# Kernel optimization log

Measured on AMD Instinct MI355X. Metric: run time of the kernel, lower is better.

## Reference

```python
import jax, jax.numpy as jnp
import numpy as np

N = 100000
E = 1600000
D = 64
NEG_SLOPE = 0.2


def setup_inputs() -> dict:
    key = jax.random.key(0)
    ks = jax.random.split(key, 16)
    inp = {}
    inp['x'] = jax.random.normal(ks[0], (N, D), dtype=jnp.float32)
    for i, name in enumerate(['edges_pos_out', 'edges_pos_in', 'edges_neg_out', 'edges_neg_in']):
        inp[name] = jax.random.randint(ks[1 + i], (2, E), 0, N, dtype=jnp.int64)
    s = 1.0 / np.sqrt(D)
    inp['gat_W'] = jax.random.normal(ks[5], (2, 4, D, D), dtype=jnp.float32) * s
    inp['gat_att_src'] = jax.random.normal(ks[6], (2, 4, D), dtype=jnp.float32) * s
    inp['gat_att_dst'] = jax.random.normal(ks[7], (2, 4, D), dtype=jnp.float32) * s
    inp['gat_bias'] = jnp.zeros((2, 4, D), dtype=jnp.float32)
    inp['mlp_W1'] = jax.random.normal(ks[8], (2, 5 * D, D), dtype=jnp.float32) * (1.0 / np.sqrt(5 * D))
    inp['mlp_b1'] = jnp.zeros((2, D), dtype=jnp.float32)
    inp['mlp_W2'] = jax.random.normal(ks[9], (2, D, D), dtype=jnp.float32) * s
    inp['mlp_b2'] = jnp.zeros((2, D), dtype=jnp.float32)
    return inp


def _gat(x, W, att_src, att_dst, bias, src, dst):
    # PyG GATConv, heads=1, add_self_loops=True
    n = x.shape[0]
    h = x @ W                                  # [N, D]
    a_src = h @ att_src                        # [N]
    a_dst = h @ att_dst                        # [N]
    loops = jnp.arange(n, dtype=src.dtype)
    s = jnp.concatenate([src, loops])
    d = jnp.concatenate([dst, loops])
    alpha = jax.nn.leaky_relu(a_src[s] + a_dst[d], NEG_SLOPE)   # [E+N]
    m = jax.ops.segment_max(alpha, d, num_segments=n)
    e = jnp.exp(alpha - m[d])
    z = jax.ops.segment_sum(e, d, num_segments=n)
    w = e / z[d]
    out = jax.ops.segment_sum(w[:, None] * h[s], d, num_segments=n)
    return out + bias


def _sdr_layer(x, edge_lists, W, a_s, a_d, b, W1, b1, W2, b2):
    feats = [x]
    for r, (src, dst) in enumerate(edge_lists):
        feats.append(_gat(x, W[r], a_s[r], a_d[r], b[r], src, dst))
    combined = jnp.concatenate(feats, axis=1)          # [N, 5D]
    hidden = jnp.tanh(combined @ W1 + b1)
    return hidden @ W2 + b2


def reference(x, edges_pos_out, edges_pos_in, edges_neg_out, edges_neg_in,
              gat_W, gat_att_src, gat_att_dst, gat_bias,
              mlp_W1, mlp_b1, mlp_W2, mlp_b2):
    edge_lists = [(e[0], e[1]) for e in
                  (edges_pos_out, edges_pos_in, edges_neg_out, edges_neg_in)]
    for l in range(gat_W.shape[0]):
        x = _sdr_layer(x, edge_lists, gat_W[l], gat_att_src[l], gat_att_dst[l],
                       gat_bias[l], mlp_W1[l], mlp_b1[l], mlp_W2[l], mlp_b2[l])
    return x
```

## Files before the change

### kernel.cpp

```cpp
#include <hip/hip_runtime.h>
#include <hip/hip_bf16.h>
#include <math.h>

#define D 64
#define NEG 0.2f
#define WPB 4
#define BLK 256
#define DPB 128
#define MAXNB 1024
#define CHUNK 16384

typedef __attribute__((ext_vector_type(8))) short bf8;
typedef __attribute__((ext_vector_type(4))) float f4;
typedef __attribute__((ext_vector_type(4))) int i4;

__device__ __forceinline__ float lrelu(float v) { return v > 0.f ? v : NEG * v; }

__device__ __forceinline__ unsigned short f2bf(float f) {
    unsigned u = __float_as_uint(f);
    u = (u + 0x7fffu + ((u >> 16) & 1u)) >> 16;
    return (unsigned short)u;
}
__device__ __forceinline__ bf8 ld_frag_g(const unsigned short* p) {
    i4 v = *(const i4*)p;
    return __builtin_bit_cast(bf8, v);
}

__device__ __forceinline__ const int* edge_ptr(const int* e0, const int* e1,
                                               const int* e2, const int* e3, int r)
{
    return (r == 0) ? e0 : (r == 1) ? e1 : (r == 2) ? e2 : e3;
}


__global__ __launch_bounds__(256) void k_bcount(
    const int* __restrict__ e0, const int* __restrict__ e1,
    const int* __restrict__ e2, const int* __restrict__ e3,
    int* __restrict__ bcnt, int E, int NB)
{
    int r = blockIdx.y;
    const int* dst = edge_ptr(e0, e1, e2, e3, r) + E;
    __shared__ int hist[MAXNB];
    for (int i = threadIdx.x; i < NB; i += 256) hist[i] = 0;
    __syncthreads();
    int base = blockIdx.x * CHUNK;
    int end = base + CHUNK < E ? base + CHUNK : E;
    for (int i = base + threadIdx.x; i < end; i += 256)
        atomicAdd(&hist[dst[i] >> 7], 1);
    __syncthreads();
    for (int i = threadIdx.x; i < NB; i += 256)
        if (hist[i]) atomicAdd(&bcnt[r * NB + i], hist[i]);
}

__global__ __launch_bounds__(1024) void k_bscan(
    const int* __restrict__ bcnt, int* __restrict__ boff,
    int* __restrict__ bcur, int* __restrict__ prefix, int E, int N, int NB)
{
    int r = blockIdx.y;
    __shared__ int sh[1024];
    int t = threadIdx.x;
    int v = (t < NB) ? bcnt[r * NB + t] : 0;
    sh[t] = v;
    __syncthreads();
    for (int off = 1; off < 1024; off <<= 1) {
        int add = (t >= off) ? sh[t - off] : 0;
        __syncthreads();
        sh[t] += add;
        __syncthreads();
    }
    if (t < NB) {
        int excl = sh[t] - v;
        boff[r * (NB + 1) + t] = excl;
        bcur[r * NB + t] = excl;
    }
    if (t == 0) {
        boff[r * (NB + 1) + NB] = E;
        prefix[(size_t)r * (N + 1) + N] = E;
    }
}

__global__ __launch_bounds__(256) void k_part(
    const int* __restrict__ e0, const int* __restrict__ e1,
    const int* __restrict__ e2, const int* __restrict__ e3,
    int* __restrict__ gcur, unsigned* __restrict__ staging, int E, int NB)
{
    int r = blockIdx.y;
    const int* ep = edge_ptr(e0, e1, e2, e3, r);
    const int* srcp = ep;
    const int* dstp = ep + E;
    __shared__ int hist[MAXNB];
    __shared__ int base[MAXNB];
    for (int j = threadIdx.x; j < NB; j += 256) hist[j] = 0;
    __syncthreads();
    int begin = blockIdx.x * CHUNK;
    int end = begin + CHUNK < E ? begin + CHUNK : E;
    for (int i = begin + threadIdx.x; i < end; i += 256)
        atomicAdd(&hist[dstp[i] >> 7], 1);
    __syncthreads();
    for (int j = threadIdx.x; j < NB; j += 256) {
        int c = hist[j];
        base[j] = c ? atomicAdd(&gcur[r * NB + j], c) : 0;
        hist[j] = 0;
    }
    __syncthreads();
    unsigned* stg = staging + (size_t)r * E;
    for (int i = begin + threadIdx.x; i < end; i += 256) {
        int d = dstp[i];
        int b = d >> 7;
        int pos = base[b] + atomicAdd(&hist[b], 1);
        stg[pos] = ((unsigned)srcp[i] << 7) | (unsigned)(d & 127);
    }
}

__global__ __launch_bounds__(256) void k_place(
    const unsigned* __restrict__ staging, const int* __restrict__ boff,
    int* __restrict__ prefix, int* __restrict__ srcs, int N, int E, int NB)
{
    int r = blockIdx.y;
    int b = blockIdx.x;
    int t = threadIdx.x;
    __shared__ int lcount[DPB];
    __shared__ int ls[DPB];
    __shared__ int lcur[DPB];
    int gbase = boff[r * (NB + 1) + b];
    int bcnt = boff[r * (NB + 1) + b + 1] - gbase;
    if (t < DPB) lcount[t] = 0;
    __syncthreads();
    const unsigned* st = staging + (size_t)r * E + gbase;
    for (int i = t; i < bcnt; i += 256)
        atomicAdd(&lcount[st[i] & 127], 1);
    __syncthreads();
    if (t < DPB) ls[t] = lcount[t];
    __syncthreads();
    for (int off = 1; off < DPB; off <<= 1) {
        int add = (t < DPB && t >= off) ? ls[t - off] : 0;
        __syncthreads();
        if (t < DPB) ls[t] += add;
        __syncthreads();
    }
    int lo = b * DPB;
    if (t < DPB) {
        int excl = ls[t] - lcount[t];
        lcur[t] = excl;
        int d = lo + t;
        if (d < N) prefix[(size_t)r * (N + 1) + d] = gbase + excl;
    }
    __syncthreads();
    for (int i = t; i < bcnt; i += 256) {
        unsigned v = st[i];
        int pos = atomicAdd(&lcur[v & 127], 1);
        srcs[(size_t)r * E + gbase + pos] = (int)(v >> 7);
    }
}


__global__ __launch_bounds__(256) void k_xcast(
    const float* __restrict__ x, unsigned short* __restrict__ xb, int n4)
{
    int i = blockIdx.x * 256 + threadIdx.x;
    if (i < n4) {
        float4 v = ((const float4*)x)[i];
        ushort4 o;
        o.x = f2bf(v.x); o.y = f2bf(v.y); o.z = f2bf(v.z); o.w = f2bf(v.w);
        ((ushort4*)xb)[i] = o;
    }
}

__global__ __launch_bounds__(64) void k_pack(
    const float* __restrict__ gatW, const float* __restrict__ atS,
    const float* __restrict__ atD, const float* __restrict__ W1,
    const float* __restrict__ W2, unsigned short* __restrict__ WgP,
    unsigned short* __restrict__ W1P, unsigned short* __restrict__ W2P)
{
    int f = blockIdx.x;
    int L = threadIdx.x;
    int kg = L >> 4, c = L & 15;
    unsigned short vals[8];
    unsigned short* dst;
    if (f < 80) {
        int m = f / 10, rem = f % 10;
        int l = m / 4, r = m % 4;
        int kc = rem / 5, ct = rem % 5;
        const float* W = gatW + (size_t)(l * 4 + r) * D * D;
        if (ct < 4) {
#pragma unroll
            for (int j = 0; j < 8; j++) {
                int k = kc * 32 + kg * 8 + j;
                vals[j] = f2bf(W[k * D + ct * 16 + c]);
            }
        } else {
            const float* att = (c == 0) ? atS + (size_t)(l * 4 + r) * D
                                        : atD + (size_t)(l * 4 + r) * D;
#pragma unroll
            for (int j = 0; j < 8; j++) {
                int k = kc * 32 + kg * 8 + j;
                float s = 0.f;
                if (c < 2)
                    for (int cc = 0; cc < D; cc++) s += W[k * D + cc] * att[cc];
                vals[j] = f2bf(s);
            }
        }
        dst = WgP + ((size_t)f * 64 + L) * 8;
    } else if (f < 160) {
        int f2 = f - 80;
        int l = f2 / 40, rem = f2 % 40;
        int kc = rem / 4, ct = rem % 4;
        const float* W = W1 + (size_t)l * 5 * D * D;
#pragma unroll
        for (int j = 0; j < 8; j++) {
            int k = kc * 32 + kg * 8 + j;
            vals[j] = f2bf(W[k * D + ct * 16 + c]);
        }
        dst = W1P + ((size_t)f2 * 64 + L) * 8;
    } else {
        int f3 = f - 160;
        int l = f3 / 8, rem = f3 % 8;
        int kc = rem / 4, ct = rem % 4;
        const float* W = W2 + (size_t)l * D * D;
#pragma unroll
        for (int j = 0; j < 8; j++) {
            int k = kc * 32 + kg * 8 + j;
            vals[j] = f2bf(W[k * D + ct * 16 + c]);
        }
        dst = W2P + ((size_t)f3 * 64 + L) * 8;
    }
    i4 v = __builtin_bit_cast(i4, *(bf8*)vals);
    *(i4*)dst = v;
}


__device__ __forceinline__ void gemm_h_body(
    bf8 a0, bf8 a1, const unsigned short* __restrict__ WgPl,
    unsigned short* __restrict__ h, float* __restrict__ a_s,
    float* __restrict__ a_d, int n0, int kg, int lo, int L, int N)
{
#pragma unroll
    for (int r = 0; r < 4; r++) {
        const unsigned short* Wbase = WgPl + (size_t)r * 10 * 512;
#pragma unroll
        for (int ct = 0; ct < 5; ct++) {
            f4 acc = {0.f, 0.f, 0.f, 0.f};
            bf8 b0 = ld_frag_g(Wbase + (size_t)ct * 512 + (size_t)L * 8);
            bf8 b1 = ld_frag_g(Wbase + (size_t)(5 + ct) * 512 + (size_t)L * 8);
            acc = __builtin_amdgcn_mfma_f32_16x16x32_bf16(a0, b0, acc, 0, 0, 0);
            acc = __builtin_amdgcn_mfma_f32_16x16x32_bf16(a1, b1, acc, 0, 0, 0);
#pragma unroll
            for (int q = 0; q < 4; q++) {
                int node = n0 + kg * 4 + q;
                if (node < N) {
                    if (ct < 4)
                        h[((size_t)r * N + node) * D + ct * 16 + lo] = f2bf(acc[q]);
                    else if (lo == 0)
                        a_s[(size_t)r * N + node] = acc[q];
                    else if (lo == 1)
                        a_d[(size_t)r * N + node] = acc[q];
                }
            }
        }
    }
}

__global__ __launch_bounds__(BLK) void k_gemm_h(
    const unsigned short* __restrict__ xb, const unsigned short* __restrict__ WgPl,
    unsigned short* __restrict__ h, float* __restrict__ a_s,
    float* __restrict__ a_d, int N)
{
    int w = threadIdx.x >> 6, L = threadIdx.x & 63;
    int n0 = blockIdx.x * 64 + w * 16;
    int lo = L & 15, kg = L >> 4;
    int nA = n0 + lo; if (nA >= N) nA = N - 1;
    bf8 a0 = ld_frag_g(xb + (size_t)nA * D + kg * 8);
    bf8 a1 = ld_frag_g(xb + (size_t)nA * D + 32 + kg * 8);
    gemm_h_body(a0, a1, WgPl, h, a_s, a_d, n0, kg, lo, L, N);
}

__global__ __launch_bounds__(BLK) void k_agg(
    const unsigned short* __restrict__ h, const float* __restrict__ a_sall,
    const float* __restrict__ a_dall, const int* __restrict__ prefix,
    const int* __restrict__ srcsall, const float* __restrict__ gatB,
    unsigned short* __restrict__ g, int N, int E)
{
    __shared__ int2 pairs[WPB][64];
    int r = blockIdx.y;
    int w = threadIdx.x >> 6, lane = threadIdx.x & 63;
    int half = lane >> 5, fl = lane & 31;
    int d = (blockIdx.x * WPB + w) * 2 + half;
    if (d >= N) d = N - 1;

    const unsigned short* hr = h + (size_t)r * N * D;
    const float* a_src = a_sall + (size_t)r * N;
    const int* starts = prefix + (size_t)r * (N + 1);
    const int* srcs = srcsall + (size_t)r * E;

    int base = starts[d];
    int cnt = starts[d + 1] - base;
    float ad = a_dall[(size_t)r * N + d];

    float e_self = __expf(lrelu(a_src[d] + ad));
    float zpart = (fl == 0) ? e_self : 0.f;
    float accx, accy;
    {
        unsigned u = ((const unsigned*)(hr + (size_t)d * D))[fl];
        accx = e_self * __uint_as_float(u << 16);
        accy = e_self * __uint_as_float(u & 0xffff0000u);
    }

    int cntmax = max(cnt, __shfl_xor(cnt, 32));
    for (int c0 = 0; c0 < cntmax; c0 += 32) {
        int jj = c0 + fl;
        bool valid = jj < cnt;
        int s = valid ? srcs[base + jj] : 0;
        float e = valid ? __expf(lrelu(a_src[s] + ad)) : 0.f;
        zpart += e;
        pairs[w][lane] = make_int2(s * (int)(D * 2), __float_as_int(e));
        __threadfence_block();
        int lim = cntmax - c0; if (lim > 32) lim = 32;
        int rlim = (lim + 3) & ~3;
#pragma unroll 2
        for (int t = 0; t < rlim; t += 2) {
            i4 pv = *(const i4*)(&pairs[w][half * 32 + t]);
            unsigned uA = *(const unsigned*)((const char*)hr + pv.x + fl * 4);
            unsigned uB = *(const unsigned*)((const char*)hr + pv.z + fl * 4);
            float eA = __int_as_float(pv.y), eB = __int_as_float(pv.w);
            accx = fmaf(eA, __uint_as_float(uA << 16), accx);
            accy = fmaf(eA, __uint_as_float(uA & 0xffff0000u), accy);
            accx = fmaf(eB, __uint_as_float(uB << 16), accx);
            accy = fmaf(eB, __uint_as_float(uB & 0xffff0000u), accy);
        }
        __threadfence_block();
    }

    float z = zpart;
#pragma unroll
    for (int off = 16; off; off >>= 1) z += __shfl_xor(z, off);

    float rz = 1.f / z;
    float vlo = accx * rz + gatB[r * D + 2 * fl];
    float vhi = accy * rz + gatB[r * D + 2 * fl + 1];
    unsigned o = (unsigned)f2bf(vlo) | ((unsigned)f2bf(vhi) << 16);
    ((unsigned*)g)[((size_t)r * N + d) * 32 + fl] = o;
}

__global__ __launch_bounds__(BLK) void k_mlp(
    const unsigned short* __restrict__ xb, const unsigned short* __restrict__ g,
    const unsigned short* __restrict__ W1Pl, const float* __restrict__ b1l,
    const unsigned short* __restrict__ W2Pl, const float* __restrict__ b2l,
    void* __restrict__ outp, int N, int last,
    const unsigned short* __restrict__ WgPn, unsigned short* __restrict__ hn,
    float* __restrict__ a_sn, float* __restrict__ a_dn)
{
    __shared__ unsigned short sh[WPB][16 * 80];
    int w = threadIdx.x >> 6, L = threadIdx.x & 63;
    int n0 = blockIdx.x * 64 + w * 16;
    int lo = L & 15, kg = L >> 4;
    int nA = n0 + lo; if (nA >= N) nA = N - 1;

    f4 acc[4];
#pragma unroll
    for (int ct = 0; ct < 4; ct++) acc[ct] = (f4){0.f, 0.f, 0.f, 0.f};

#pragma unroll
    for (int p = 0; p < 5; p++) {
        const unsigned short* plane = (p == 0) ? xb : g + (size_t)(p - 1) * N * D;
#pragma unroll
        for (int kc2 = 0; kc2 < 2; kc2++) {
            bf8 a = ld_frag_g(plane + (size_t)nA * D + kc2 * 32 + kg * 8);
            int kc = p * 2 + kc2;
#pragma unroll
            for (int ct = 0; ct < 4; ct++) {
                bf8 b = ld_frag_g(W1Pl + ((size_t)(kc * 4 + ct) * 512 + (size_t)L * 8));
                acc[ct] = __builtin_amdgcn_mfma_f32_16x16x32_bf16(a, b, acc[ct], 0, 0, 0);
            }
        }
    }

    unsigned short* tile = &sh[w][0];
#pragma unroll
    for (int ct = 0; ct < 4; ct++) {
        float bb = b1l[ct * 16 + lo];
#pragma unroll
        for (int q = 0; q < 4; q++)
            tile[(kg * 4 + q) * 80 + ct * 16 + lo] = f2bf(tanhf(acc[ct][q] + bb));
    }
    __syncthreads();

    f4 o[4];
#pragma unroll
    for (int ct = 0; ct < 4; ct++) o[ct] = (f4){0.f, 0.f, 0.f, 0.f};
#pragma unroll
    for (int kc = 0; kc < 2; kc++) {
        const unsigned short* ap = tile + lo * 80 + kc * 32 + kg * 8;
        i4 av = *(const i4*)ap;
        bf8 a = __builtin_bit_cast(bf8, av);
#pragma unroll
        for (int ct = 0; ct < 4; ct++) {
            bf8 b = ld_frag_g(W2Pl + ((size_t)(kc * 4 + ct) * 512 + (size_t)L * 8));
            o[ct] = __builtin_amdgcn_mfma_f32_16x16x32_bf16(a, b, o[ct], 0, 0, 0);
        }
    }
    __syncthreads();
#pragma unroll
    for (int ct = 0; ct < 4; ct++) {
        float bb = b2l[ct * 16 + lo];
#pragma unroll
        for (int q = 0; q < 4; q++) {
            int node = n0 + kg * 4 + q;
            int col = ct * 16 + lo;
            float v = o[ct][q] + bb;
            if (node < N) {
                if (last) ((float*)outp)[(size_t)node * D + col] = v;
                else ((unsigned short*)outp)[(size_t)node * D + col] = f2bf(v);
            }
            if (!last) tile[(kg * 4 + q) * 80 + col] = f2bf(v);
        }
    }
    if (last) return;

    __syncthreads();
    bf8 a0, a1;
    {
        i4 v0 = *(const i4*)(tile + lo * 80 + kg * 8);
        i4 v1 = *(const i4*)(tile + lo * 80 + 32 + kg * 8);
        a0 = __builtin_bit_cast(bf8, v0);
        a1 = __builtin_bit_cast(bf8, v1);
    }
    gemm_h_body(a0, a1, WgPn, hn, a_sn, a_dn, n0, kg, lo, L, N);
}


extern "C" void kernel_launch(void* const* d_in, const int* in_sizes, int n_in,
                              void* d_out, int out_size, void* d_ws, size_t ws_size,
                              hipStream_t stream)
{
    const float* x    = (const float*)d_in[0];
    const int*   e0   = (const int*)d_in[1];
    const int*   e1   = (const int*)d_in[2];
    const int*   e2   = (const int*)d_in[3];
    const int*   e3   = (const int*)d_in[4];
    const float* gatW = (const float*)d_in[5];
    const float* atS  = (const float*)d_in[6];
    const float* atD  = (const float*)d_in[7];
    const float* gatB = (const float*)d_in[8];
    const float* W1   = (const float*)d_in[9];
    const float* b1   = (const float*)d_in[10];
    const float* W2   = (const float*)d_in[11];
    const float* b2   = (const float*)d_in[12];
    float* out = (float*)d_out;

    const int N = in_sizes[0] / D;
    const int E = in_sizes[1] / 2;
    const int NB = (N + DPB - 1) / DPB;

    size_t off = 0;
    auto alloc = [&](size_t bytes) { size_t o = off; off = (off + bytes + 255) & ~(size_t)255; return o; };
    unsigned short* xb    = (unsigned short*)((char*)d_ws + alloc((size_t)N * D * 2));
    unsigned short* xnext = (unsigned short*)((char*)d_ws + alloc((size_t)N * D * 2));
    unsigned short* h     = (unsigned short*)((char*)d_ws + alloc((size_t)4 * N * D * 2));
    unsigned short* g     = (unsigned short*)((char*)d_ws + alloc((size_t)4 * N * D * 2));
    unsigned* staging = (unsigned*)g;
    float* a_s   = (float*)((char*)d_ws + alloc((size_t)4 * N * 4));
    float* a_d   = (float*)((char*)d_ws + alloc((size_t)4 * N * 4));
    int* prefix  = (int*)((char*)d_ws + alloc((size_t)4 * (N + 1) * 4));
    int* srcs    = (int*)((char*)d_ws + alloc((size_t)4 * E * 4));
    int* bcnt    = (int*)((char*)d_ws + alloc((size_t)4 * NB * 4));
    int* boff    = (int*)((char*)d_ws + alloc((size_t)4 * (NB + 1) * 4));
    int* bcur    = (int*)((char*)d_ws + alloc((size_t)4 * NB * 4));
    unsigned short* WgP = (unsigned short*)((char*)d_ws + alloc((size_t)80 * 512 * 2));
    unsigned short* W1P = (unsigned short*)((char*)d_ws + alloc((size_t)80 * 512 * 2));
    unsigned short* W2P = (unsigned short*)((char*)d_ws + alloc((size_t)16 * 512 * 2));
    (void)ws_size;

    const int partBlocks = (E + CHUNK - 1) / CHUNK;
    const int tileBlocks = (N + 63) / 64;
    const int aggBlocks  = (N + 8 * 1 - 1) / 8;

    k_pack<<<176, 64, 0, stream>>>(gatW, atS, atD, W1, W2, WgP, W1P, W2P);
    k_xcast<<<(N * D / 4 + 255) / 256, 256, 0, stream>>>(x, xb, N * D / 4);

    hipMemsetAsync(bcnt, 0, (size_t)4 * NB * 4, stream);
    k_bcount<<<dim3(partBlocks, 4), 256, 0, stream>>>(e0, e1, e2, e3, bcnt, E, NB);
    k_bscan<<<dim3(1, 4), 1024, 0, stream>>>(bcnt, boff, bcur, prefix, E, N, NB);
    k_part<<<dim3(partBlocks, 4), 256, 0, stream>>>(e0, e1, e2, e3, bcur, staging, E, NB);
    k_place<<<dim3(NB, 4), 256, 0, stream>>>(staging, boff, prefix, srcs, N, E, NB);

    k_gemm_h<<<tileBlocks, BLK, 0, stream>>>(xb, WgP, h, a_s, a_d, N);
    k_agg<<<dim3(aggBlocks, 4), BLK, 0, stream>>>(
        h, a_s, a_d, prefix, srcs, gatB, g, N, E);
    k_mlp<<<tileBlocks, BLK, 0, stream>>>(
        xb, g, W1P, b1, W2P, b2, xnext, N, 0,
        WgP + (size_t)40 * 512, h, a_s, a_d);

    k_agg<<<dim3(aggBlocks, 4), BLK, 0, stream>>>(
        h, a_s, a_d, prefix, srcs, gatB + (size_t)4 * D, g, N, E);
    k_mlp<<<tileBlocks, BLK, 0, stream>>>(
        xnext, g, W1P + (size_t)40 * 512, b1 + D, W2P + (size_t)8 * 512, b2 + D,
        out, N, 1, nullptr, nullptr, nullptr, nullptr);
}
```

Before: 686.0 us.

## Stage partitioned edges in shared memory for coalesced bucket scatter; unroll aggregation loop

The partition kernel now does a local counting sort of each chunk into shared memory (prefix scan of the bucket histogram, then local placement). It then writes to the global staging buffer in sorted order, so writes to the same bucket land contiguously instead of being scattered. The chunk is halved so the staging arrays fit in shared memory, which doubles the number of partition blocks and the global atomics. The aggregation inner loop is also unrolled further, with the trip count padded to a multiple of 8.

After: 594.5 us. 13.3% less time.

```diff
diff --git a/kernel.cpp b/kernel.cpp
--- a/kernel.cpp
+++ b/kernel.cpp
@@ -9,6 +9,7 @@
 #define DPB 128
 #define MAXNB 1024
 #define CHUNK 16384
+#define PCHUNK 8192
 
 typedef __attribute__((ext_vector_type(8))) short bf8;
 typedef __attribute__((ext_vector_type(4))) float f4;
@@ -84,32 +85,62 @@
     const int* __restrict__ e2, const int* __restrict__ e3,
     int* __restrict__ gcur, unsigned* __restrict__ staging, int E, int NB)
 {
+    __shared__ unsigned vals[PCHUNK];
+    __shared__ unsigned short bkt[PCHUNK];
+    __shared__ int hist[MAXNB];
+    __shared__ int sbase[MAXNB];
+    __shared__ int gdelta[MAXNB];
+    __shared__ int ssum[256];
     int r = blockIdx.y;
     const int* ep = edge_ptr(e0, e1, e2, e3, r);
     const int* srcp = ep;
     const int* dstp = ep + E;
-    __shared__ int hist[MAXNB];
-    __shared__ int base[MAXNB];
-    for (int j = threadIdx.x; j < NB; j += 256) hist[j] = 0;
-    __syncthreads();
-    int begin = blockIdx.x * CHUNK;
-    int end = begin + CHUNK < E ? begin + CHUNK : E;
-    for (int i = begin + threadIdx.x; i < end; i += 256)
+    int t = threadIdx.x;
+    for (int j = t; j < MAXNB; j += 256) hist[j] = 0;
+    __syncthreads();
+    int begin = blockIdx.x * PCHUNK;
+    int end = begin + PCHUNK < E ? begin + PCHUNK : E;
+    int cnt = end - begin;
+    for (int i = begin + t; i < end; i += 256)
         atomicAdd(&hist[dstp[i] >> 7], 1);
     __syncthreads();
-    for (int j = threadIdx.x; j < NB; j += 256) {
+    int h0 = hist[t * 4], h1 = hist[t * 4 + 1], h2 = hist[t * 4 + 2], h3 = hist[t * 4 + 3];
+    int lsum = h0 + h1 + h2 + h3;
+    ssum[t] = lsum;
+    __syncthreads();
+    for (int off = 1; off < 256; off <<= 1) {
+        int a = (t >= off) ? ssum[t - off] : 0;
+        __syncthreads();
+        ssum[t] += a;
+        __syncthreads();
+    }
+    int ex = ssum[t] - lsum;
+    sbase[t * 4] = ex;
+    sbase[t * 4 + 1] = ex + h0;
+    sbase[t * 4 + 2] = ex + h0 + h1;
+    sbase[t * 4 + 3] = ex + h0 + h1 + h2;
+    __syncthreads();
+    for (int j = t; j < NB; j += 256) {
         int c = hist[j];
-        base[j] = c ? atomicAdd(&gcur[r * NB + j], c) : 0;
-        hist[j] = 0;
+        int gb = c ? atomicAdd(&gcur[r * NB + j], c) : 0;
+        gdelta[j] = gb - sbase[j];
+    }
+    __syncthreads();
+    for (int j = t; j < MAXNB; j += 256) hist[j] = 0;
+    __syncthreads();
+    for (int i = begin + t; i < end; i += 256) {
+        int d = dstp[i];
+        int s = srcp[i];
+        int b = d >> 7;
+        int rank = atomicAdd(&hist[b], 1);
+        int p = sbase[b] + rank;
+        vals[p] = ((unsigned)s << 7) | (unsigned)(d & 127);
+        bkt[p] = (unsigned short)b;
     }
     __syncthreads();
     unsigned* stg = staging + (size_t)r * E;
-    for (int i = begin + threadIdx.x; i < end; i += 256) {
-        int d = dstp[i];
-        int b = d >> 7;
-        int pos = base[b] + atomicAdd(&hist[b], 1);
-        stg[pos] = ((unsigned)srcp[i] << 7) | (unsigned)(d & 127);
-    }
+    for (int p = t; p < cnt; p += 256)
+        stg[p + gdelta[bkt[p]]] = vals[p];
 }
 
 __global__ __launch_bounds__(256) void k_place(
@@ -315,8 +346,8 @@
         pairs[w][lane] = make_int2(s * (int)(D * 2), __float_as_int(e));
         __threadfence_block();
         int lim = cntmax - c0; if (lim > 32) lim = 32;
-        int rlim = (lim + 3) & ~3;
-#pragma unroll 2
+        int rlim = (lim + 7) & ~7;
+#pragma unroll 4
         for (int t = 0; t < rlim; t += 2) {
             i4 pv = *(const i4*)(&pairs[w][half * 32 + t]);
             unsigned uA = *(const unsigned*)((const char*)hr + pv.x + fl * 4);
@@ -470,15 +501,16 @@
     unsigned short* W2P = (unsigned short*)((char*)d_ws + alloc((size_t)16 * 512 * 2));
     (void)ws_size;
 
-    const int partBlocks = (E + CHUNK - 1) / CHUNK;
+    const int cntBlocks  = (E + CHUNK - 1) / CHUNK;
+    const int partBlocks = (E + PCHUNK - 1) / PCHUNK;
     const int tileBlocks = (N + 63) / 64;
-    const int aggBlocks  = (N + 8 * 1 - 1) / 8;
+    const int aggBlocks  = (N + 7) / 8;
 
     k_pack<<<176, 64, 0, stream>>>(gatW, atS, atD, W1, W2, WgP, W1P, W2P);
     k_xcast<<<(N * D / 4 + 255) / 256, 256, 0, stream>>>(x, xb, N * D / 4);
 
     hipMemsetAsync(bcnt, 0, (size_t)4 * NB * 4, stream);
-    k_bcount<<<dim3(partBlocks, 4), 256, 0, stream>>>(e0, e1, e2, e3, bcnt, E, NB);
+    k_bcount<<<dim3(cntBlocks, 4), 256, 0, stream>>>(e0, e1, e2, e3, bcnt, E, NB);
     k_bscan<<<dim3(1, 4), 1024, 0, stream>>>(bcnt, boff, bcur, prefix, E, N, NB);
     k_part<<<dim3(partBlocks, 4), 256, 0, stream>>>(e0, e1, e2, e3, bcur, staging, E, NB);
     k_place<<<dim3(NB, 4), 256, 0, stream>>>(staging, boff, prefix, srcs, N, E, NB);
```
